# Kernel optimization log

Hardware: AMD Instinct MI355X
Metric: run time of the kernel (lower is better)

## Reference

```python
import jax, jax.numpy as jnp
import numpy as np
import math

HIDDEN = 768
HEADS = 12
HEAD_DIM = HIDDEN // HEADS  # 64
SEQ = 197
K_RANK = min(128, HEAD_DIM)  # 64
BATCH = 64


def setup_inputs() -> dict:
    key = jax.random.key(0)
    ks = jax.random.split(key, 12)
    init = 0.02
    # Linear weights stored [in, out] (equivalent to torch W.T)
    return {
        "hidden_states": jax.random.normal(ks[0], (BATCH, SEQ, HIDDEN), dtype=jnp.float32),
        "Wq": jax.random.normal(ks[1], (HIDDEN, HIDDEN), dtype=jnp.float32) * init,
        "bq": jnp.zeros((HIDDEN,), dtype=jnp.float32),
        "Wk": jax.random.normal(ks[2], (HIDDEN, HIDDEN), dtype=jnp.float32) * init,
        "bk": jnp.zeros((HIDDEN,), dtype=jnp.float32),
        "Wv": jax.random.normal(ks[3], (HIDDEN, HIDDEN), dtype=jnp.float32) * init,
        "bv": jnp.zeros((HIDDEN,), dtype=jnp.float32),
        "Wo": jax.random.normal(ks[4], (HIDDEN, HIDDEN), dtype=jnp.float32) * init,
        "bo": jnp.zeros((HIDDEN,), dtype=jnp.float32),
        "E_k": jax.random.normal(ks[5], (SEQ, K_RANK), dtype=jnp.float32) * init,
        "E_v": jax.random.normal(ks[6], (SEQ, K_RANK), dtype=jnp.float32) * init,
    }


def reference(hidden_states, Wq, bq, Wk, bk, Wv, bv, Wo, bo, E_k, E_v):
    B, S, D = hidden_states.shape
    H, d = HEADS, HEAD_DIM
    scale = 1.0 / math.sqrt(d)

    def split_heads(x):  # [B,S,D] -> [B,H,S,d]
        return x.reshape(B, S, H, d).transpose(0, 2, 1, 3)

    q = split_heads(hidden_states @ Wq + bq)
    k = split_heads(hidden_states @ Wk + bk)
    v = split_heads(hidden_states @ Wv + bv)

    # low-rank projection of K/V along the sequence axis: [B,H,k,d]
    pk = jnp.einsum('sk,bhsd->bhkd', E_k, k)
    pv = jnp.einsum('sk,bhsd->bhkd', E_v, v)

    # scores over reduced axis: [B,H,S,k]
    scores = jnp.einsum('bhsd,bhkd->bhsk', q, pk) * scale
    probs = jax.nn.softmax(scores, axis=-1)

    ctx = jnp.einsum('bhsk,bhkd->bhsd', probs, pv)
    ctx = ctx.transpose(0, 2, 1, 3).reshape(B, S, D)
    out = ctx @ Wo + bo  # dropout rate 0.0 -> identity
    return out
```

## Files before the change

### kernel.cpp

```cpp
#include <hip/hip_runtime.h>
#include <math.h>

#define B_   64
#define S_   197
#define D_   768
#define H_   12
#define HD_  64
#define M_   (B_ * S_)
#define MPAD 12672
#define KE   224
#define BH_  (B_ * H_)
#define WSZ  ((size_t)D_ * D_)

typedef _Float16 half8_t __attribute__((ext_vector_type(8)));
typedef _Float16 half4_t __attribute__((ext_vector_type(4)));
typedef _Float16 half2_t __attribute__((ext_vector_type(2)));
typedef float floatx4 __attribute__((ext_vector_type(4)));

#define LDS_DMA16(gptr, lptr) \
  __builtin_amdgcn_global_load_lds((const __attribute__((address_space(1))) void*)(gptr), \
                                   (__attribute__((address_space(3))) void*)(lptr), 16, 0, 0)

__global__ __launch_bounds__(256) void prep_kernel(
    const float* __restrict__ X,
    const float* __restrict__ Wq, const float* __restrict__ Wk,
    const float* __restrict__ Wv, const float* __restrict__ Wo,
    const float* __restrict__ Ek, const float* __restrict__ Ev,
    _Float16* __restrict__ Xh,
    _Float16* __restrict__ Tcat, _Float16* __restrict__ To,
    _Float16* __restrict__ EET,
    float* __restrict__ esumK, float* __restrict__ esumV)
{
    __shared__ float tile[32][33];
    const int bid = blockIdx.x, tid = threadIdx.x;
    if (bid < 9504) {
        const int i4 = (bid * 256 + tid) * 4;
        float4 v = make_float4(0.f, 0.f, 0.f, 0.f);
        if (i4 < M_ * D_) v = *(const float4*)&X[i4];
        half4_t o = { (_Float16)v.x, (_Float16)v.y, (_Float16)v.z, (_Float16)v.w };
        *(half4_t*)&Xh[i4] = o;
        return;
    }
    int b2 = bid - 9504;
    if (b2 < 2304) {
        const int z = b2 / 576, rem = b2 % 576;
        const int bx = rem % 24, by = rem / 24;
        const float* W = (z == 0) ? Wk : (z == 1) ? Wv : (z == 2) ? Wq : Wo;
        _Float16* T = (z < 3) ? (Tcat + (size_t)z * WSZ) : To;
        const int n0 = bx * 32, k0 = by * 32;
        const int r = tid >> 3, c4 = (tid & 7) * 4;
        *(float4*)&tile[r][c4] = *(const float4*)&W[(size_t)(k0 + r) * D_ + n0 + c4];
        __syncthreads();
        half4_t o = { (_Float16)tile[c4 + 0][r], (_Float16)tile[c4 + 1][r],
                      (_Float16)tile[c4 + 2][r], (_Float16)tile[c4 + 3][r] };
        *(half4_t*)&T[(size_t)(n0 + r) * D_ + k0 + c4] = o;
        return;
    }
    b2 -= 2304;
    const float* E = b2 ? Ev : Ek;
    _Float16* ET = EET + (size_t)b2 * 64 * KE;
    float* es = b2 ? esumV : esumK;
    for (int i = tid; i < 64 * KE; i += 256) {
        const int rr = i / KE, s = i % KE;
        ET[i] = (_Float16)((s < S_) ? E[s * 64 + rr] : 0.f);
    }
    if (tid < 64) {
        float acc = 0.f;
        for (int s = 0; s < S_; ++s) acc += E[s * 64 + tid];
        es[tid] = acc;
    }
}

__global__ __launch_bounds__(256) void y_kernel(
    const _Float16* __restrict__ Xh, const _Float16* __restrict__ EET,
    _Float16* __restrict__ Ybuf)
{
    __shared__ _Float16 Xs[KE * 66];
    const int bid = blockIdx.x;
    const int b = bid / 12, n0 = (bid % 12) * 64;
    const int tid = threadIdx.x, w = tid >> 6, lane = tid & 63;
    const int l15 = lane & 15, quad = lane >> 4;

    #pragma unroll
    for (int i = 0; i < 7; ++i) {
        const int s = i * 32 + (tid >> 3);
        const int d0 = (tid & 7) * 8;
        const half8_t v = *(const half8_t*)&Xh[(size_t)(b * S_ + s) * D_ + n0 + d0];
        #pragma unroll
        for (int jj = 0; jj < 4; ++jj) {
            half2_t t2 = { v[2 * jj], v[2 * jj + 1] };
            *(half2_t*)&Xs[s * 66 + d0 + 2 * jj] = t2;
        }
    }
    __syncthreads();

    floatx4 acc[2][4] = {};
    #pragma unroll
    for (int k7 = 0; k7 < 7; ++k7) {
        half8_t af[2];
        #pragma unroll
        for (int mi = 0; mi < 2; ++mi)
            af[mi] = *(const half8_t*)&EET[(w * 32 + mi * 16 + l15) * KE + k7 * 32 + quad * 8];
        #pragma unroll
        for (int ni = 0; ni < 4; ++ni) {
            const int sb = k7 * 32 + quad * 8;
            half8_t bf;
            #pragma unroll
            for (int jj = 0; jj < 8; ++jj) bf[jj] = Xs[(sb + jj) * 66 + ni * 16 + l15];
            #pragma unroll
            for (int mi = 0; mi < 2; ++mi)
                acc[mi][ni] = __builtin_amdgcn_mfma_f32_16x16x32_f16(
                    af[mi], bf, acc[mi][ni], 0, 0, 0);
        }
    }

    #pragma unroll
    for (int mi = 0; mi < 2; ++mi)
        #pragma unroll
        for (int ni = 0; ni < 4; ++ni)
            #pragma unroll
            for (int i = 0; i < 4; ++i) {
                const int m_local = w * 32 + mi * 16 + quad * 4 + i;
                const int row = (m_local >> 6) * 4096 + b * 64 + (m_local & 63);
                Ybuf[(size_t)row * D_ + n0 + ni * 16 + l15] = (_Float16)acc[mi][ni][i];
            }
}

__global__ __launch_bounds__(256) void gemm_qpkv(
    const _Float16* __restrict__ Xh, const _Float16* __restrict__ Ybuf,
    const _Float16* __restrict__ Tcat,
    const float* __restrict__ bq, const float* __restrict__ bk,
    const float* __restrict__ bv,
    const float* __restrict__ esumK, const float* __restrict__ esumV,
    _Float16* __restrict__ Qh, _Float16* __restrict__ pk16,
    _Float16* __restrict__ pv16)
{
    __shared__ _Float16 sm[16384];
    const int bid = blockIdx.x;
    const _Float16 *A, *W;
    const float *bias, *esum;
    _Float16* O16;
    int m0, n0, rowb;
    if (bid < 624) {
        const int xcd = bid & 7, t = bid >> 3;
        const int slot = t / 6, j = t - slot * 6;
        const int m_blk = slot * 8 + xcd;
        if (m_blk >= MPAD / 128) return;
        m0 = m_blk * 128; n0 = j * 128; rowb = m0;
        A = Xh; W = Tcat + 2 * WSZ + (size_t)n0 * D_;
        bias = bq; esum = nullptr; O16 = Qh;
    } else {
        const int b2 = bid - 624;
        const int xcd = b2 & 7, t = b2 >> 3;
        const int slot = t / 6, j = t - slot * 6;
        const int m_blk = slot * 8 + xcd;
        m0 = m_blk * 128; n0 = j * 128;
        const bool pv = (m_blk >= 32);
        rowb = pv ? m0 - 4096 : m0;
        A = Ybuf; W = Tcat + (pv ? WSZ : 0) + (size_t)n0 * D_;
        bias = pv ? bv : bk; esum = pv ? esumV : esumK;
        O16 = pv ? pv16 : pk16;
    }

    const int tid = threadIdx.x;
    const int w = tid >> 6, lane = tid & 63;
    const int fr = lane & 15, quad = lane >> 4, f7 = lane & 7;
    const int l3 = lane >> 3;
    const int csrc = ((lane & 7) ^ l3) * 8;
    const int wm = (w >> 1) * 64, wn = (w & 1) * 64;

    const _Float16* Abase = A + (size_t)(m0 + w * 32 + l3) * D_ + csrc;
    const _Float16* Wbase = W + (size_t)(w * 32 + l3) * D_ + csrc;

    floatx4 acc[4][4] = {};

    for (int k0 = 0; k0 < D_; k0 += 64) {
        #pragma unroll
        for (int j = 0; j < 4; ++j) {
            LDS_DMA16(Abase + (size_t)(j * 8) * D_ + k0, &sm[w * 2048 + j * 512]);
            LDS_DMA16(Wbase + (size_t)(j * 8) * D_ + k0, &sm[8192 + w * 2048 + j * 512]);
        }
        __syncthreads();
        #pragma unroll
        for (int ksub = 0; ksub < 2; ++ksub) {
            const int sa = ((ksub * 4 + quad) ^ f7) * 8;
            half8_t af[4], bf[4];
            #pragma unroll
            for (int i = 0; i < 4; ++i) {
                af[i] = *(const half8_t*)&sm[(wm + i * 16 + fr) * 64 + sa];
                bf[i] = *(const half8_t*)&sm[8192 + (wn + i * 16 + fr) * 64 + sa];
            }
            #pragma unroll
            for (int mi = 0; mi < 4; ++mi)
                #pragma unroll
                for (int ni = 0; ni < 4; ++ni)
                    acc[mi][ni] = __builtin_amdgcn_mfma_f32_16x16x32_f16(
                        af[mi], bf[ni], acc[mi][ni], 0, 0, 0);
        }
        __syncthreads();
    }

    float bval[4];
    #pragma unroll
    for (int ni = 0; ni < 4; ++ni)
        bval[ni] = bias[n0 + wn + ni * 16 + fr];

    _Float16* ct = &sm[w * 2176];
    #pragma unroll
    for (int half = 0; half < 2; ++half) {
        #pragma unroll
        for (int mi2 = 0; mi2 < 2; ++mi2) {
            const int mi = half * 2 + mi2;
            float esv[4] = {1.f, 1.f, 1.f, 1.f};
            if (esum) {
                const float4 es4 = *(const float4*)&esum[mi * 16 + quad * 4];
                esv[0] = es4.x; esv[1] = es4.y; esv[2] = es4.z; esv[3] = es4.w;
            }
            #pragma unroll
            for (int ni = 0; ni < 4; ++ni)
                #pragma unroll
                for (int i = 0; i < 4; ++i)
                    ct[(mi2 * 16 + quad * 4 + i) * 68 + ni * 16 + fr] =
                        (_Float16)(acc[mi][ni][i] + esv[i] * bval[ni]);
        }
        #pragma unroll
        for (int pass = 0; pass < 4; ++pass) {
            const int rr = pass * 8 + (lane >> 3);
            const int cc = (lane & 7) * 8;
            const half8_t v = *(const half8_t*)&ct[rr * 68 + cc];
            *(half8_t*)&O16[(size_t)(rowb + wm + half * 32 + rr) * D_ + n0 + wn + cc] = v;
        }
    }
}

__global__ __launch_bounds__(256) void gemm_o(
    const _Float16* __restrict__ CTX, const _Float16* __restrict__ To,
    const float* __restrict__ bo, float* __restrict__ O32)
{
    __shared__ _Float16 sm[12288];
    const int xcd = blockIdx.x & 7, t = blockIdx.x >> 3;
    const int slot = t / 6, j = t - slot * 6;
    const int m_blk = slot * 8 + xcd;
    if (m_blk >= MPAD / 64) return;
    const int m0 = m_blk * 64, n0 = j * 128;

    const int tid = threadIdx.x;
    const int w = tid >> 6, lane = tid & 63;
    const int fr = lane & 15, quad = lane >> 4, f7 = lane & 7;
    const int l3 = lane >> 3;
    const int csrc = ((lane & 7) ^ l3) * 8;
    const int wm = (w >> 1) * 32, wn = (w & 1) * 64;

    const _Float16* Abase = CTX + (size_t)(m0 + w * 16 + l3) * D_ + csrc;
    const _Float16* Wbase = To + (size_t)(n0 + w * 32 + l3) * D_ + csrc;

    floatx4 acc[2][4] = {};

    for (int k0 = 0; k0 < D_; k0 += 64) {
        #pragma unroll
        for (int j2 = 0; j2 < 2; ++j2)
            LDS_DMA16(Abase + (size_t)(j2 * 8) * D_ + k0, &sm[w * 1024 + j2 * 512]);
        #pragma unroll
        for (int j2 = 0; j2 < 4; ++j2)
            LDS_DMA16(Wbase + (size_t)(j2 * 8) * D_ + k0, &sm[4096 + w * 2048 + j2 * 512]);
        __syncthreads();
        #pragma unroll
        for (int ksub = 0; ksub < 2; ++ksub) {
            const int sa = ((ksub * 4 + quad) ^ f7) * 8;
            half8_t af[2], bf[4];
            #pragma unroll
            for (int i = 0; i < 2; ++i)
                af[i] = *(const half8_t*)&sm[(wm + i * 16 + fr) * 64 + sa];
            #pragma unroll
            for (int i = 0; i < 4; ++i)
                bf[i] = *(const half8_t*)&sm[4096 + (wn + i * 16 + fr) * 64 + sa];
            #pragma unroll
            for (int mi = 0; mi < 2; ++mi)
                #pragma unroll
                for (int ni = 0; ni < 4; ++ni)
                    acc[mi][ni] = __builtin_amdgcn_mfma_f32_16x16x32_f16(
                        af[mi], bf[ni], acc[mi][ni], 0, 0, 0);
        }
        __syncthreads();
    }

    float bval[4];
    #pragma unroll
    for (int ni = 0; ni < 4; ++ni)
        bval[ni] = bo[n0 + wn + ni * 16 + fr];

    const int rq = quad * 4;
    if (m0 + 64 <= M_) {
        #pragma unroll
        for (int ni = 0; ni < 4; ++ni) {
            const int n = n0 + wn + ni * 16 + fr;
            #pragma unroll
            for (int mi = 0; mi < 2; ++mi)
                #pragma unroll
                for (int i = 0; i < 4; ++i)
                    O32[(size_t)(m0 + wm + mi * 16 + rq + i) * D_ + n] =
                        acc[mi][ni][i] + bval[ni];
        }
    } else {
        #pragma unroll
        for (int ni = 0; ni < 4; ++ni) {
            const int n = n0 + wn + ni * 16 + fr;
            #pragma unroll
            for (int mi = 0; mi < 2; ++mi)
                #pragma unroll
                for (int i = 0; i < 4; ++i) {
                    const int m = m0 + wm + mi * 16 + rq + i;
                    if (m < M_)
                        O32[(size_t)m * D_ + n] = acc[mi][ni][i] + bval[ni];
                }
        }
    }
}

__global__ __launch_bounds__(256) void attn_kernel(
    const _Float16* __restrict__ Qh, const _Float16* __restrict__ pk16,
    const _Float16* __restrict__ pv16, _Float16* __restrict__ CTXh)
{
    __shared__ _Float16 P[64 * 80];
    const int bh = blockIdx.x, b = bh / H_, h = bh % H_;
    const int tid = threadIdx.x, w = tid >> 6, lane = tid & 63;
    const int l15 = lane & 15, quad = lane >> 4;
    const _Float16* pkB = pk16 + (size_t)(b * 64) * D_ + h * 64;
    const _Float16* pvB = pv16 + (size_t)(b * 64) * D_ + h * 64;
    const size_t qbase = (size_t)(b * S_) * D_ + h * HD_;

    half8_t bkf[4][2], bvf[4][2];
    #pragma unroll
    for (int ni = 0; ni < 4; ++ni)
        #pragma unroll
        for (int kk = 0; kk < 2; ++kk) {
            bkf[ni][kk] = *(const half8_t*)&pkB[(size_t)(ni * 16 + l15) * D_ + kk * 32 + quad * 8];
            #pragma unroll
            for (int jj = 0; jj < 8; ++jj)
                bvf[ni][kk][jj] = pvB[(size_t)(kk * 32 + quad * 8 + jj) * D_ + ni * 16 + l15];
        }

    for (int t = w; t < 13; t += 4) {
        const int srow = t * 16;
        floatx4 acc[4] = {};
        #pragma unroll
        for (int kk = 0; kk < 2; ++kk) {
            const half8_t aq = *(const half8_t*)
                &Qh[qbase + (size_t)(srow + l15) * D_ + kk * 32 + quad * 8];
            #pragma unroll
            for (int ni = 0; ni < 4; ++ni)
                acc[ni] = __builtin_amdgcn_mfma_f32_16x16x32_f16(
                    aq, bkf[ni][kk], acc[ni], 0, 0, 0);
        }
        float p[4][4];
        #pragma unroll
        for (int i = 0; i < 4; ++i) {
            const float s0 = acc[0][i] * 0.125f, s1 = acc[1][i] * 0.125f;
            const float s2 = acc[2][i] * 0.125f, s3 = acc[3][i] * 0.125f;
            float mx = fmaxf(fmaxf(s0, s1), fmaxf(s2, s3));
            #pragma unroll
            for (int off = 1; off < 16; off <<= 1)
                mx = fmaxf(mx, __shfl_xor(mx, off, 64));
            const float e0 = __expf(s0 - mx), e1 = __expf(s1 - mx);
            const float e2 = __expf(s2 - mx), e3 = __expf(s3 - mx);
            float sme = e0 + e1 + e2 + e3;
            #pragma unroll
            for (int off = 1; off < 16; off <<= 1)
                sme += __shfl_xor(sme, off, 64);
            const float inv = 1.f / sme;
            p[0][i] = e0 * inv; p[1][i] = e1 * inv;
            p[2][i] = e2 * inv; p[3][i] = e3 * inv;
        }
        #pragma unroll
        for (int ni = 0; ni < 4; ++ni)
            #pragma unroll
            for (int i = 0; i < 4; ++i)
                P[(w * 16 + quad * 4 + i) * 80 + ni * 16 + l15] = (_Float16)p[ni][i];

        floatx4 accv[4] = {};
        #pragma unroll
        for (int kk = 0; kk < 2; ++kk) {
            const half8_t ap = *(const half8_t*)&P[(w * 16 + l15) * 80 + kk * 32 + quad * 8];
            #pragma unroll
            for (int ni = 0; ni < 4; ++ni)
                accv[ni] = __builtin_amdgcn_mfma_f32_16x16x32_f16(
                    ap, bvf[ni][kk], accv[ni], 0, 0, 0);
        }
        #pragma unroll
        for (int ni = 0; ni < 4; ++ni)
            #pragma unroll
            for (int i = 0; i < 4; ++i) {
                const int s = srow + quad * 4 + i;
                if (s < S_)
                    CTXh[qbase + (size_t)s * D_ + ni * 16 + l15] = (_Float16)accv[ni][i];
            }
    }
}

extern "C" void kernel_launch(void* const* d_in, const int* in_sizes, int n_in,
                              void* d_out, int out_size, void* d_ws, size_t ws_size,
                              hipStream_t stream) {
    const float* X   = (const float*)d_in[0];
    const float* Wq  = (const float*)d_in[1];
    const float* bq  = (const float*)d_in[2];
    const float* Wk  = (const float*)d_in[3];
    const float* bk  = (const float*)d_in[4];
    const float* Wv  = (const float*)d_in[5];
    const float* bv  = (const float*)d_in[6];
    const float* Wo  = (const float*)d_in[7];
    const float* bo  = (const float*)d_in[8];
    const float* E_k = (const float*)d_in[9];
    const float* E_v = (const float*)d_in[10];
    float* out = (float*)d_out;

    char* p = (char*)d_ws;
    _Float16* Xh   = (_Float16*)p; p += (size_t)MPAD * D_ * 2;
    _Float16* Tcat = (_Float16*)p; p += (size_t)3 * WSZ * 2;
    _Float16* To   = (_Float16*)p; p += (size_t)WSZ * 2;
    _Float16* Qh   = (_Float16*)p; p += (size_t)MPAD * D_ * 2;
    _Float16* EET  = (_Float16*)p; p += (size_t)128 * KE * 2;
    float* esumK   = (float*)p;    p += 64 * sizeof(float);
    float* esumV   = (float*)p;    p += 64 * sizeof(float);
    _Float16* Ybuf = (_Float16*)p; p += (size_t)8192 * D_ * 2;
    _Float16* pk16 = (_Float16*)p; p += (size_t)4096 * D_ * 2;
    _Float16* pv16 = (_Float16*)p;

    prep_kernel<<<11810, 256, 0, stream>>>(X, Wq, Wk, Wv, Wo, E_k, E_v,
                                           Xh, Tcat, To, EET, esumK, esumV);
    y_kernel<<<768, 256, 0, stream>>>(Xh, EET, Ybuf);
    gemm_qpkv<<<1008, 256, 0, stream>>>(Xh, Ybuf, Tcat,
                                        bq, bk, bv, esumK, esumV,
                                        Qh, pk16, pv16);
    attn_kernel<<<BH_, 256, 0, stream>>>(Qh, pk16, pv16, Xh);
    gemm_o<<<1200, 256, 0, stream>>>(Xh, To, bo, out);
}
```

Before: 209.2 us.

## Fuse Y projection into prep kernel and enlarge output GEMM tile to 128x128

Merges the y_kernel into the prep kernel. Y blocks are interleaved with the fp16 conversion blocks and read X and E_k/E_v directly in fp32, which removes one launch and the EET staging buffer. The output projection GEMM tile grows from 64x128 to 128x128 with 4x4 MFMA accumulators per wave, halving the grid to raise data reuse per block. The trade-offs are more registers per thread, fewer blocks to fill the CUs, and strided uncoalesced fp32 reads of E inside the MFMA loop.

Result: no change. 209.4 us (+0.1%).

```diff
diff --git a/kernel.cpp b/kernel.cpp
--- a/kernel.cpp
+++ b/kernel.cpp
@@ -21,29 +21,40 @@
   __builtin_amdgcn_global_load_lds((const __attribute__((address_space(1))) void*)(gptr), \
                                    (__attribute__((address_space(3))) void*)(lptr), 16, 0, 0)
 
-__global__ __launch_bounds__(256) void prep_kernel(
+__global__ __launch_bounds__(256) void prep_y_kernel(
     const float* __restrict__ X,
     const float* __restrict__ Wq, const float* __restrict__ Wk,
     const float* __restrict__ Wv, const float* __restrict__ Wo,
     const float* __restrict__ Ek, const float* __restrict__ Ev,
     _Float16* __restrict__ Xh,
     _Float16* __restrict__ Tcat, _Float16* __restrict__ To,
-    _Float16* __restrict__ EET,
-    float* __restrict__ esumK, float* __restrict__ esumV)
+    float* __restrict__ esumK, float* __restrict__ esumV,
+    _Float16* __restrict__ Ybuf)
 {
-    __shared__ float tile[32][33];
+    __shared__ _Float16 smem[KE * 66];
     const int bid = blockIdx.x, tid = threadIdx.x;
-    if (bid < 9504) {
-        const int i4 = (bid * 256 + tid) * 4;
+
+    int task, idx;
+    if (bid < 9984) {
+        const int q = bid / 13, r = bid - q * 13;
+        if (r == 0) { task = 0; idx = q; }
+        else        { task = 1; idx = 12 * q + r - 1; }
+    } else if (bid < 10272) { task = 1; idx = 9216 + (bid - 9984); }
+    else if (bid < 12576)   { task = 2; idx = bid - 10272; }
+    else                    { task = 3; idx = bid - 12576; }
+
+    if (task == 1) {
+        const int i4 = (idx * 256 + tid) * 4;
         float4 v = make_float4(0.f, 0.f, 0.f, 0.f);
         if (i4 < M_ * D_) v = *(const float4*)&X[i4];
         half4_t o = { (_Float16)v.x, (_Float16)v.y, (_Float16)v.z, (_Float16)v.w };
         *(half4_t*)&Xh[i4] = o;
         return;
     }
-    int b2 = bid - 9504;
-    if (b2 < 2304) {
-        const int z = b2 / 576, rem = b2 % 576;
+
+    if (task == 2) {
+        float (*tile)[33] = (float (*)[33])smem;
+        const int z = idx / 576, rem = idx % 576;
         const int bx = rem % 24, by = rem / 24;
         const float* W = (z == 0) ? Wk : (z == 1) ? Wv : (z == 2) ? Wq : Wo;
         _Float16* T = (z < 3) ? (Tcat + (size_t)z * WSZ) : To;
@@ -56,39 +67,39 @@
         *(half4_t*)&T[(size_t)(n0 + r) * D_ + k0 + c4] = o;
         return;
     }
-    b2 -= 2304;
-    const float* E = b2 ? Ev : Ek;
-    _Float16* ET = EET + (size_t)b2 * 64 * KE;
-    float* es = b2 ? esumV : esumK;
-    for (int i = tid; i < 64 * KE; i += 256) {
-        const int rr = i / KE, s = i % KE;
-        ET[i] = (_Float16)((s < S_) ? E[s * 64 + rr] : 0.f);
-    }
-    if (tid < 64) {
-        float acc = 0.f;
-        for (int s = 0; s < S_; ++s) acc += E[s * 64 + tid];
-        es[tid] = acc;
-    }
-}
-
-__global__ __launch_bounds__(256) void y_kernel(
-    const _Float16* __restrict__ Xh, const _Float16* __restrict__ EET,
-    _Float16* __restrict__ Ybuf)
-{
-    __shared__ _Float16 Xs[KE * 66];
-    const int bid = blockIdx.x;
-    const int b = bid / 12, n0 = (bid % 12) * 64;
-    const int tid = threadIdx.x, w = tid >> 6, lane = tid & 63;
+
+    if (task == 3) {
+        const float* E = idx ? Ev : Ek;
+        float* es = idx ? esumV : esumK;
+        if (tid < 64) {
+            float acc = 0.f;
+            for (int s = 0; s < S_; ++s) acc += E[s * 64 + tid];
+            es[tid] = acc;
+        }
+        return;
+    }
+
+    _Float16* Xs = smem;
+    const int b = idx / 12, n0 = (idx % 12) * 64;
+    const int w = tid >> 6, lane = tid & 63;
     const int l15 = lane & 15, quad = lane >> 4;
 
     #pragma unroll
     for (int i = 0; i < 7; ++i) {
         const int s = i * 32 + (tid >> 3);
         const int d0 = (tid & 7) * 8;
-        const half8_t v = *(const half8_t*)&Xh[(size_t)(b * S_ + s) * D_ + n0 + d0];
+        float4 v0 = make_float4(0.f, 0.f, 0.f, 0.f), v1 = v0;
+        if (s < S_) {
+            const float* src = &X[(size_t)(b * S_ + s) * D_ + n0 + d0];
+            v0 = *(const float4*)src;
+            v1 = *(const float4*)(src + 4);
+        }
+        const _Float16 h[8] = { (_Float16)v0.x, (_Float16)v0.y, (_Float16)v0.z,
+                                (_Float16)v0.w, (_Float16)v1.x, (_Float16)v1.y,
+                                (_Float16)v1.z, (_Float16)v1.w };
         #pragma unroll
         for (int jj = 0; jj < 4; ++jj) {
-            half2_t t2 = { v[2 * jj], v[2 * jj + 1] };
+            half2_t t2 = { h[2 * jj], h[2 * jj + 1] };
             *(half2_t*)&Xs[s * 66 + d0 + 2 * jj] = t2;
         }
     }
@@ -99,8 +110,16 @@
     for (int k7 = 0; k7 < 7; ++k7) {
         half8_t af[2];
         #pragma unroll
-        for (int mi = 0; mi < 2; ++mi)
-            af[mi] = *(const half8_t*)&EET[(w * 32 + mi * 16 + l15) * KE + k7 * 32 + quad * 8];
+        for (int mi = 0; mi < 2; ++mi) {
+            const int row = w * 32 + mi * 16 + l15;
+            const float* Esrc = (row < 64) ? Ek : Ev;
+            const int er = row & 63;
+            #pragma unroll
+            for (int jj = 0; jj < 8; ++jj) {
+                const int s = k7 * 32 + quad * 8 + jj;
+                af[mi][jj] = (_Float16)((s < S_) ? Esrc[s * 64 + er] : 0.f);
+            }
+        }
         #pragma unroll
         for (int ni = 0; ni < 4; ++ni) {
             const int sb = k7 * 32 + quad * 8;
@@ -237,45 +256,43 @@
     const _Float16* __restrict__ CTX, const _Float16* __restrict__ To,
     const float* __restrict__ bo, float* __restrict__ O32)
 {
-    __shared__ _Float16 sm[12288];
+    __shared__ _Float16 sm[16384];
     const int xcd = blockIdx.x & 7, t = blockIdx.x >> 3;
     const int slot = t / 6, j = t - slot * 6;
     const int m_blk = slot * 8 + xcd;
-    if (m_blk >= MPAD / 64) return;
-    const int m0 = m_blk * 64, n0 = j * 128;
+    if (m_blk >= MPAD / 128) return;
+    const int m0 = m_blk * 128, n0 = j * 128;
 
     const int tid = threadIdx.x;
     const int w = tid >> 6, lane = tid & 63;
     const int fr = lane & 15, quad = lane >> 4, f7 = lane & 7;
     const int l3 = lane >> 3;
     const int csrc = ((lane & 7) ^ l3) * 8;
-    const int wm = (w >> 1) * 32, wn = (w & 1) * 64;
-
-    const _Float16* Abase = CTX + (size_t)(m0 + w * 16 + l3) * D_ + csrc;
+    const int wm = (w >> 1) * 64, wn = (w & 1) * 64;
+
+    const _Float16* Abase = CTX + (size_t)(m0 + w * 32 + l3) * D_ + csrc;
     const _Float16* Wbase = To + (size_t)(n0 + w * 32 + l3) * D_ + csrc;
 
-    floatx4 acc[2][4] = {};
+    floatx4 acc[4][4] = {};
 
     for (int k0 = 0; k0 < D_; k0 += 64) {
         #pragma unroll
-        for (int j2 = 0; j2 < 2; ++j2)
-            LDS_DMA16(Abase + (size_t)(j2 * 8) * D_ + k0, &sm[w * 1024 + j2 * 512]);
-        #pragma unroll
-        for (int j2 = 0; j2 < 4; ++j2)
-            LDS_DMA16(Wbase + (size_t)(j2 * 8) * D_ + k0, &sm[4096 + w * 2048 + j2 * 512]);
+        for (int j2 = 0; j2 < 4; ++j2) {
+            LDS_DMA16(Abase + (size_t)(j2 * 8) * D_ + k0, &sm[w * 2048 + j2 * 512]);
+            LDS_DMA16(Wbase + (size_t)(j2 * 8) * D_ + k0, &sm[8192 + w * 2048 + j2 * 512]);
+        }
         __syncthreads();
         #pragma unroll
         for (int ksub = 0; ksub < 2; ++ksub) {
             const int sa = ((ksub * 4 + quad) ^ f7) * 8;
-            half8_t af[2], bf[4];
-            #pragma unroll
-            for (int i = 0; i < 2; ++i)
+            half8_t af[4], bf[4];
+            #pragma unroll
+            for (int i = 0; i < 4; ++i) {
                 af[i] = *(const half8_t*)&sm[(wm + i * 16 + fr) * 64 + sa];
-            #pragma unroll
-            for (int i = 0; i < 4; ++i)
-                bf[i] = *(const half8_t*)&sm[4096 + (wn + i * 16 + fr) * 64 + sa];
-            #pragma unroll
-            for (int mi = 0; mi < 2; ++mi)
+                bf[i] = *(const half8_t*)&sm[8192 + (wn + i * 16 + fr) * 64 + sa];
+            }
+            #pragma unroll
+            for (int mi = 0; mi < 4; ++mi)
                 #pragma unroll
                 for (int ni = 0; ni < 4; ++ni)
                     acc[mi][ni] = __builtin_amdgcn_mfma_f32_16x16x32_f16(
@@ -289,31 +306,18 @@
     for (int ni = 0; ni < 4; ++ni)
         bval[ni] = bo[n0 + wn + ni * 16 + fr];
 
-    const int rq = quad * 4;
-    if (m0 + 64 <= M_) {
-        #pragma unroll
-        for (int ni = 0; ni < 4; ++ni) {
-            const int n = n0 + wn + ni * 16 + fr;
-            #pragma unroll
-            for (int mi = 0; mi < 2; ++mi)
-                #pragma unroll
-                for (int i = 0; i < 4; ++i)
-                    O32[(size_t)(m0 + wm + mi * 16 + rq + i) * D_ + n] =
-                        acc[mi][ni][i] + bval[ni];
-        }
-    } else {
-        #pragma unroll
-        for (int ni = 0; ni < 4; ++ni) {
-            const int n = n0 + wn + ni * 16 + fr;
-            #pragma unroll
-            for (int mi = 0; mi < 2; ++mi)
-                #pragma unroll
-                for (int i = 0; i < 4; ++i) {
-                    const int m = m0 + wm + mi * 16 + rq + i;
-                    if (m < M_)
-                        O32[(size_t)m * D_ + n] = acc[mi][ni][i] + bval[ni];
-                }
-        }
+    const bool full = (m0 + 128 <= M_);
+    #pragma unroll
+    for (int ni = 0; ni < 4; ++ni) {
+        const int n = n0 + wn + ni * 16 + fr;
+        #pragma unroll
+        for (int mi = 0; mi < 4; ++mi)
+            #pragma unroll
+            for (int i = 0; i < 4; ++i) {
+                const int m = m0 + wm + mi * 16 + quad * 4 + i;
+                if (full || m < M_)
+                    O32[(size_t)m * D_ + n] = acc[mi][ni][i] + bval[ni];
+            }
     }
 }
 
@@ -418,19 +422,17 @@
     _Float16* Tcat = (_Float16*)p; p += (size_t)3 * WSZ * 2;
     _Float16* To   = (_Float16*)p; p += (size_t)WSZ * 2;
     _Float16* Qh   = (_Float16*)p; p += (size_t)MPAD * D_ * 2;
-    _Float16* EET  = (_Float16*)p; p += (size_t)128 * KE * 2;
     float* esumK   = (float*)p;    p += 64 * sizeof(float);
     float* esumV   = (float*)p;    p += 64 * sizeof(float);
     _Float16* Ybuf = (_Float16*)p; p += (size_t)8192 * D_ * 2;
     _Float16* pk16 = (_Float16*)p; p += (size_t)4096 * D_ * 2;
     _Float16* pv16 = (_Float16*)p;
 
-    prep_kernel<<<11810, 256, 0, stream>>>(X, Wq, Wk, Wv, Wo, E_k, E_v,
-                                           Xh, Tcat, To, EET, esumK, esumV);
-    y_kernel<<<768, 256, 0, stream>>>(Xh, EET, Ybuf);
+    prep_y_kernel<<<12578, 256, 0, stream>>>(X, Wq, Wk, Wv, Wo, E_k, E_v,
+                                             Xh, Tcat, To, esumK, esumV, Ybuf);
     gemm_qpkv<<<1008, 256, 0, stream>>>(Xh, Ybuf, Tcat,
                                         bq, bk, bv, esumK, esumV,
                                         Qh, pk16, pv16);
     attn_kernel<<<BH_, 256, 0, stream>>>(Qh, pk16, pv16, Xh);
-    gemm_o<<<1200, 256, 0, stream>>>(Xh, To, bo, out);
+    gemm_o<<<624, 256, 0, stream>>>(Xh, To, bo, out);
 }
```
